# Kernel tuning notes

Hardware: AMD Instinct MI355X
Metric: run time of the kernel (lower is better)

The kernel has to match this reference:

```python
import jax, jax.numpy as jnp
import numpy as np

N_NODES = 500000
N_EDGES = 600000
N_GRAPHS = 4096
X_DIM = 128
H_DIM = 128
Z_DIM = 64
BN_EPS = 1e-5


def setup_inputs() -> dict:
    key = jax.random.key(0)
    ks = jax.random.split(key, 16)
    inp = {
        'x': jax.random.normal(ks[0], (N_NODES, X_DIM), dtype=jnp.float32),
        'edge_index': jax.random.randint(ks[1], (2, N_EDGES), 0, N_NODES),
        'edge_weights': jax.random.uniform(ks[2], (N_EDGES,), dtype=jnp.float32),
        'y_target': jax.random.uniform(ks[3], (N_GRAPHS, 1), dtype=jnp.float32),
        'batch': jnp.sort(jax.random.randint(ks[4], (N_NODES,), 0, N_GRAPHS)),
        # embedder (single weighted GCN-style layer) params
        'W_self': jax.random.normal(ks[5], (X_DIM, H_DIM), dtype=jnp.float32) / np.sqrt(X_DIM),
        'W_nbr': jax.random.normal(ks[6], (X_DIM, H_DIM), dtype=jnp.float32) / np.sqrt(X_DIM),
        'b_emb': jnp.zeros((H_DIM,), dtype=jnp.float32),
        # encoder_mean head: Linear(h_dim+1, z_dim) + BatchNorm1d(z_dim) + ReLU
        'W_mu': jax.random.normal(ks[7], (H_DIM + 1, Z_DIM), dtype=jnp.float32) / np.sqrt(H_DIM + 1),
        'b_mu': jnp.zeros((Z_DIM,), dtype=jnp.float32),
        'gamma_mu': jnp.ones((Z_DIM,), dtype=jnp.float32),
        'beta_mu': jnp.zeros((Z_DIM,), dtype=jnp.float32),
        # encoder_var head: Linear + BN + ReLU + Sigmoid
        'W_var': jax.random.normal(ks[8], (H_DIM + 1, Z_DIM), dtype=jnp.float32) / np.sqrt(H_DIM + 1),
        'b_var': jnp.zeros((Z_DIM,), dtype=jnp.float32),
        'gamma_var': jnp.ones((Z_DIM,), dtype=jnp.float32),
        'beta_var': jnp.zeros((Z_DIM,), dtype=jnp.float32),
    }
    return inp


def _batchnorm(a, gamma, beta):
    # BatchNorm1d in training mode: per-feature batch stats (biased var)
    mu = jnp.mean(a, axis=0, keepdims=True)
    var = jnp.mean((a - mu) ** 2, axis=0, keepdims=True)
    return (a - mu) * jax.lax.rsqrt(var + BN_EPS) * gamma + beta


def reference(x, edge_index, edge_weights, y_target, batch,
              W_self, W_nbr, b_emb,
              W_mu, b_mu, gamma_mu, beta_mu,
              W_var, b_var, gamma_var, beta_var):
    src, dst = edge_index[0], edge_index[1]
    # embedder.embedding(x, edge_index, edge_weights): weighted neighbor agg + self
    msg = jax.ops.segment_sum(edge_weights[:, None] * x[src], dst, num_segments=N_NODES)
    embed = jax.nn.relu(x @ W_self + msg @ W_nbr + b_emb)  # [N, H]
    # global_mean_pool over graph ids
    sums = jax.ops.segment_sum(embed, batch, num_segments=N_GRAPHS)      # [G, H]
    counts = jax.ops.segment_sum(jnp.ones((embed.shape[0],), embed.dtype), batch,
                                 num_segments=N_GRAPHS)
    graph_emb = sums / jnp.maximum(counts, 1.0)[:, None]
    # concat y_target -> [G, H+1]
    h = jnp.concatenate([graph_emb, y_target], axis=1)
    z_mu = jax.nn.relu(_batchnorm(h @ W_mu + b_mu, gamma_mu, beta_mu))
    z_logvar = jax.nn.sigmoid(jax.nn.relu(_batchnorm(h @ W_var + b_var, gamma_var, beta_var)))
    return (z_mu, z_logvar)
```

## Files before the change

kernel.cpp:

```cpp
#include <hip/hip_runtime.h>
#include <hip/hip_bf16.h>
#include <stdint.h>

#define N_NODES 500000
#define N_EDGES 600000
#define N_GRAPHS 4096
#define XD 128
#define HD 128
#define ZD 64
#define BROWS 64
#define NBUCKETS 7813
#define CAP 120

#define OFF_CURS   0ull
#define OFF_SUMS   8192ull
#define OFF_DEG    532480ull
#define OFF_NINFO  1032704ull
#define OFF_CURSOR 1532928ull
#define OFF_SBUF   2033152ull
#define OFF_AT     3909120ull
#define OFF_STATS  4433408ull
#define OFF_WT     4433664ull
#define OFF_GMEAN  4450048ull
#define OFF_PART   4974336ull
#define OFF_PAY    12974848ull

typedef __attribute__((ext_vector_type(8))) short bf16x8;
typedef __attribute__((ext_vector_type(4))) float f32x4;

__device__ inline uint32_t pk_bf16(float lo, float hi) {
  uint32_t ul = __float_as_uint(lo); ul += 0x7fffu + ((ul >> 16) & 1u);
  uint32_t uh = __float_as_uint(hi); uh += 0x7fffu + ((uh >> 16) & 1u);
  return (ul >> 16) | (uh & 0xffff0000u);
}
__device__ inline float bl16(uint32_t u) { return __uint_as_float(u << 16); }
__device__ inline float bh16(uint32_t u) { return __uint_as_float(u & 0xffff0000u); }

__global__ void wprep_kernel(const float* __restrict__ Wnbr, const float* __restrict__ Wself,
                             uint32_t* __restrict__ wt) {
  const float* __restrict__ W = blockIdx.x ? Wself : Wnbr;
  uint32_t* __restrict__ out = wt + (size_t)blockIdx.x * 8192;
  const int t = threadIdx.x;
  const int n = t >> 1, h = t & 1;
  for (int q = 0; q < 32; ++q) {
    int k2 = h * 32 + q;
    float lo = W[(2 * k2) * HD + n];
    float hi = W[(2 * k2 + 1) * HD + n];
    out[n * 64 + k2] = pk_bf16(lo, hi);
  }
}

__global__ void deg_count(const int* __restrict__ ei, uint32_t* __restrict__ deg) {
  int e = blockIdx.x * blockDim.x + threadIdx.x;
  if (e >= N_EDGES) return;
  atomicAdd(deg + ei[N_EDGES + e], 1u);
}

__global__ void scan_prefix(const uint32_t* __restrict__ deg, uint32_t* __restrict__ nodeinfo,
                            uint32_t* __restrict__ cursor) {
  const int b = blockIdx.x;
  const int lane = threadIdx.x;
  int n = b * BROWS + lane;
  int d = (n < N_NODES) ? (int)deg[n] : 0;
  int s = d;
#pragma unroll
  for (int off = 1; off < 64; off <<= 1) {
    int t = __shfl_up(s, off, 64);
    if (lane >= off) s += t;
  }
  int excl = s - d;
  int st = excl < CAP ? excl : CAP;
  int en = (excl + d) < CAP ? (excl + d) : CAP;
  if (n < N_NODES) {
    nodeinfo[n] = (uint32_t)st | ((uint32_t)en << 8);
    cursor[n] = 0u;
  }
}

__global__ void bucket_fill(const int* __restrict__ ei, const float* __restrict__ ew,
                            const uint32_t* __restrict__ nodeinfo, uint32_t* __restrict__ cursor,
                            int* __restrict__ cur_s, uint2* __restrict__ sbuf,
                            uint32_t* __restrict__ payload) {
  int e = blockIdx.x * blockDim.x + threadIdx.x;
  if (e >= N_EDGES) return;
  int src = ei[e];
  int dst = ei[N_EDGES + e];
  float w = ew[e];
  uint32_t info = nodeinfo[dst];
  int st = (int)(info & 0xffu), en = (int)((info >> 8) & 0xffu);
  int slot = (int)atomicAdd(cursor + dst, 1u);
  int pin = st + slot;
  if (pin >= en) return;
  uint32_t pos = (uint32_t)((dst >> 6) * CAP + pin);
  int bs = src >> 6;
  int ss = atomicAdd(cur_s + bs, 1);
  if (ss < CAP) {
    sbuf[(size_t)bs * CAP + ss] =
        make_uint2(((uint32_t)(src & 63) << 20) | pos, __float_as_uint(w));
  } else {
    uint4 z = make_uint4(0, 0, 0, 0);
    uint4* p = (uint4*)((char*)payload + (size_t)pos * 256);
#pragma unroll
    for (int i = 0; i < 16; ++i) p[i] = z;
  }
}

__launch_bounds__(512, 4)
__global__ void gemm_scatter(const float* __restrict__ x, const uint32_t* __restrict__ wt,
                             const uint2* __restrict__ sbuf, const int* __restrict__ cur_s,
                             uint32_t* __restrict__ payload) {
  __shared__ char lb[33728];
  uint2* srec = (uint2*)(lb + 32768);
  const int b = blockIdx.x;
  const int tid = threadIdx.x;
  const int node0 = b * BROWS;
  const int l = tid & 63, w = tid >> 6;
  const int wm = w >> 2, wn = w & 3;
  const int lr = l & 15, lk = l >> 4;

  {
    const int row = tid >> 3, c8 = tid & 7;
    int m = node0 + row;
    int mc = m < N_NODES ? m : N_NODES - 1;
    const float* xr = x + (size_t)mc * XD + c8 * 16;
    uint32_t p[8];
#pragma unroll
    for (int i = 0; i < 4; ++i) {
      float4 t4 = *(const float4*)(xr + i * 4);
      p[2 * i]     = pk_bf16(t4.x, t4.y);
      p[2 * i + 1] = pk_bf16(t4.z, t4.w);
    }
    char* aw = lb + row * 256;
    const int s0 = c8 * 2;
    *(uint4*)(aw + (((s0)     ^ (row & 7)) << 4)) = make_uint4(p[0], p[1], p[2], p[3]);
    *(uint4*)(aw + (((s0 + 1) ^ (row & 7)) << 4)) = make_uint4(p[4], p[5], p[6], p[7]);
  }
  if (tid < CAP) srec[tid] = sbuf[(size_t)b * CAP + tid];
  __syncthreads();

  f32x4 acc0[2][2];
#pragma unroll
  for (int mf = 0; mf < 2; ++mf) { acc0[mf][0] = (f32x4)0.f; acc0[mf][1] = (f32x4)0.f; }

  {
    const char* wtb = (const char*)wt;
#pragma unroll
    for (int kb = 0; kb < 4; ++kb) {
      int slot = (kb << 2) | lk;
      bf16x8 bf0 = *(const bf16x8*)(wtb + (wn * 32 + lr) * 256 + (kb << 6) + (lk << 4));
      bf16x8 bf1 = *(const bf16x8*)(wtb + (wn * 32 + 16 + lr) * 256 + (kb << 6) + (lk << 4));
#pragma unroll
      for (int mf = 0; mf < 2; ++mf) {
        int r = wm * 32 + mf * 16 + lr;
        bf16x8 a = *(const bf16x8*)(lb + r * 256 + ((slot ^ (r & 7)) << 4));
        acc0[mf][0] = __builtin_amdgcn_mfma_f32_16x16x32_bf16(a, bf0, acc0[mf][0], 0, 0, 0);
        acc0[mf][1] = __builtin_amdgcn_mfma_f32_16x16x32_bf16(a, bf1, acc0[mf][1], 0, 0, 0);
      }
    }
  }
  __syncthreads();

  {
#pragma unroll
    for (int mf = 0; mf < 2; ++mf)
#pragma unroll
      for (int nf = 0; nf < 2; ++nf) {
        int col = wn * 32 + nf * 16 + lr;
#pragma unroll
        for (int r = 0; r < 4; ++r) {
          int row = wm * 32 + mf * 16 + lk * 4 + r;
          uint32_t uv = __float_as_uint(acc0[mf][nf][r]);
          uv += 0x7fffu + ((uv >> 16) & 1u);
          *(unsigned short*)(lb + 16384 + row * 256 + ((col * 2) ^ ((row & 7) << 4))) =
              (unsigned short)(uv >> 16);
        }
      }
  }
  __syncthreads();

  {
    int cnt = cur_s[b]; if (cnt > CAP) cnt = CAP;
    const int eg = tid >> 5;
    const int c = tid & 31;
#pragma unroll
    for (int k = 0; k < 8; ++k) {
      int s = eg + (k << 4);
      if (s < cnt) {
        uint2 rec = srec[s];
        int srcloc = (int)(rec.x >> 20);
        uint32_t pos = rec.x & 0xFFFFFu;
        float wgt = __uint_as_float(rec.y);
        uint2 uv = *(const uint2*)(lb + 16384 + srcloc * 256 + ((c * 8) ^ ((srcloc & 7) << 4)));
        float a0 = bl16(uv.x) * wgt, a1 = bh16(uv.x) * wgt;
        float a2 = bl16(uv.y) * wgt, a3 = bh16(uv.y) * wgt;
        *(uint2*)((char*)payload + (size_t)pos * 256 + c * 8) =
            make_uint2(pk_bf16(a0, a1), pk_bf16(a2, a3));
      }
    }
  }
}

__launch_bounds__(512, 3)
__global__ void accum_pool(const float* __restrict__ x, const uint32_t* __restrict__ payload,
                           const uint32_t* __restrict__ nodeinfo,
                           const uint32_t* __restrict__ wt, const float* __restrict__ bemb,
                           const int* __restrict__ batch,
                           float* __restrict__ partials, float* __restrict__ sums) {
  __shared__ float lds[13376];
  float* msg = lds;
  char* astage = (char*)(lds + 8192);
  float* P = lds + 12288;
  int* span = (int*)(lds + 13312);
  const int b = blockIdx.x;
  const int tid = threadIdx.x;
  const int node0 = b * BROWS;
  const int gfirst = batch[node0];
  const int grp = tid >> 5, c = tid & 31;
  const int l = tid & 63, w = tid >> 6;
  const int wm = w >> 2, wn = w & 3;
  const int lr = l & 15, lk = l >> 4;

  for (int i = tid; i < 1024; i += 512) P[i] = 0.f;
  if (tid < 64) {
    int m = node0 + tid;
    span[tid] = (m < N_NODES) ? (batch[m] - gfirst) : -1;
  }

  {
    float acc[4][4];
#pragma unroll
    for (int rr = 0; rr < 4; ++rr)
#pragma unroll
      for (int j = 0; j < 4; ++j) acc[rr][j] = 0.f;

#pragma unroll
    for (int rr = 0; rr < 4; ++rr) {
      int row = grp * 4 + rr;
      int n = node0 + row;
      uint32_t info = (n < N_NODES) ? nodeinfo[n] : 0u;
      int st = (int)(info & 0xffu), en = (int)((info >> 8) & 0xffu);
      for (int i = st; i < en; ++i) {
        uint2 pv = *(const uint2*)(payload + ((size_t)b * CAP + i) * 64 + (c << 1));
        acc[rr][0] += bl16(pv.x);
        acc[rr][1] += bh16(pv.x);
        acc[rr][2] += bl16(pv.y);
        acc[rr][3] += bh16(pv.y);
      }
    }
#pragma unroll
    for (int rr = 0; rr < 4; ++rr) {
      int row = grp * 4 + rr;
      *(float4*)&msg[row * 128 + 4 * (c ^ (row & 7))] =
          make_float4(acc[rr][0], acc[rr][1], acc[rr][2], acc[rr][3]);
    }
  }

  {
    const int row = tid >> 3, c8 = tid & 7;
    int m = node0 + row;
    int mc = m < N_NODES ? m : N_NODES - 1;
    const float* xr = x + (size_t)mc * XD + c8 * 16;
    uint32_t p[8];
#pragma unroll
    for (int i = 0; i < 4; ++i) {
      float4 t4 = *(const float4*)(xr + i * 4);
      p[2 * i]     = pk_bf16(t4.x, t4.y);
      p[2 * i + 1] = pk_bf16(t4.z, t4.w);
    }
    char* aw = astage + row * 256;
    const int s0 = c8 * 2;
    *(uint4*)(aw + (((s0)     ^ (row & 7)) << 4)) = make_uint4(p[0], p[1], p[2], p[3]);
    *(uint4*)(aw + (((s0 + 1) ^ (row & 7)) << 4)) = make_uint4(p[4], p[5], p[6], p[7]);
  }
  __syncthreads();

  f32x4 acc1[2][2];
#pragma unroll
  for (int mf = 0; mf < 2; ++mf) { acc1[mf][0] = (f32x4)0.f; acc1[mf][1] = (f32x4)0.f; }
  {
    const char* wtb = (const char*)wt + 32768;
#pragma unroll
    for (int kb = 0; kb < 4; ++kb) {
      int slot = (kb << 2) | lk;
      bf16x8 bf0 = *(const bf16x8*)(wtb + (wn * 32 + lr) * 256 + (kb << 6) + (lk << 4));
      bf16x8 bf1 = *(const bf16x8*)(wtb + (wn * 32 + 16 + lr) * 256 + (kb << 6) + (lk << 4));
#pragma unroll
      for (int mf = 0; mf < 2; ++mf) {
        int r = wm * 32 + mf * 16 + lr;
        bf16x8 a = *(const bf16x8*)(astage + r * 256 + ((slot ^ (r & 7)) << 4));
        acc1[mf][0] = __builtin_amdgcn_mfma_f32_16x16x32_bf16(a, bf0, acc1[mf][0], 0, 0, 0);
        acc1[mf][1] = __builtin_amdgcn_mfma_f32_16x16x32_bf16(a, bf1, acc1[mf][1], 0, 0, 0);
      }
    }
  }

  {
    float be0 = bemb[wn * 32 + lr];
    float be1 = bemb[wn * 32 + 16 + lr];
#pragma unroll
    for (int mf = 0; mf < 2; ++mf)
#pragma unroll
      for (int r = 0; r < 4; ++r) {
        int row = wm * 32 + mf * 16 + lk * 4 + r;
        int xr = (row & 7) << 2;
        int i0 = row * 128 + ((wn * 32 + lr) ^ xr);
        int i1 = row * 128 + ((wn * 32 + 16 + lr) ^ xr);
        msg[i0] = fmaxf(msg[i0] + acc1[mf][0][r] + be0, 0.f);
        msg[i1] = fmaxf(msg[i1] + acc1[mf][1][r] + be1, 0.f);
      }
  }
  __syncthreads();

  if (tid < 128) {
    const int col = tid;
    float pacc = 0.f;
    int jcur = -1;
    for (int row = 0; row < 64; ++row) {
      int j = span[row];
      if (j != jcur) {
        if (jcur >= 0) {
          if (jcur < 8) P[jcur * 128 + col] = pacc;
          else atomicAdd(&sums[(size_t)(gfirst + jcur) * HD + col], pacc);
        }
        pacc = 0.f; jcur = j;
      }
      if (j >= 0) pacc += msg[row * 128 + (col ^ ((row & 7) << 2))];
    }
    if (jcur >= 0) {
      if (jcur < 8) P[jcur * 128 + col] = pacc;
      else atomicAdd(&sums[(size_t)(gfirst + jcur) * HD + col], pacc);
    }
  }
  __syncthreads();

  {
    float2 v = *(float2*)&P[tid * 2];
    *(float2*)(partials + (size_t)b * 1024 + tid * 2) = v;
  }
}

__global__ void reduce_mean(const float* __restrict__ partials, const float* __restrict__ sums,
                            const int* __restrict__ batch, float* __restrict__ gmean) {
  const int g = blockIdx.x;
  const int t = threadIdx.x;
  int lo = 0, hi = N_NODES;
  while (lo < hi) { int mid = (lo + hi) >> 1; if (batch[mid] < g) lo = mid + 1; else hi = mid; }
  int s = lo; hi = N_NODES;
  while (lo < hi) { int mid = (lo + hi) >> 1; if (batch[mid] < g + 1) lo = mid + 1; else hi = mid; }
  int e = lo;
  float tot = sums[(size_t)g * HD + t];
  int cnt = e - s;
  if (cnt > 0) {
    int b0 = s >> 6, b1 = (e - 1) >> 6;
    for (int b = b0; b <= b1; ++b) {
      int j = g - batch[b * 64];
      if (j >= 0 && j < 8) tot += partials[(size_t)b * 1024 + j * 128 + t];
    }
  }
  gmean[(size_t)g * HD + t] = tot / fmaxf((float)cnt, 1.f);
}

__global__ void head_kernel(const float* __restrict__ gmean, const float* __restrict__ y,
                            const float* __restrict__ Wmu, const float* __restrict__ bmu,
                            const float* __restrict__ Wvar, const float* __restrict__ bvar,
                            float* __restrict__ aT) {
  __shared__ float hrow[129];
  const int g = blockIdx.x;
  const int t = threadIdx.x;
  hrow[t] = gmean[(size_t)g * HD + t];
  if (t == 0) hrow[128] = y[g];
  __syncthreads();
  const int head = t >> 6, n = t & 63;
  const float* __restrict__ W = head ? Wvar : Wmu;
  float acc = head ? bvar[n] : bmu[n];
  for (int k = 0; k < 129; ++k) acc = fmaf(hrow[k], W[k * ZD + n], acc);
  aT[(size_t)(head * ZD + n) * N_GRAPHS + g] = acc;
}

__global__ void bnstats_kernel(const float* __restrict__ aT, float* __restrict__ stats) {
  const int f = blockIdx.x;
  const float* base = aT + (size_t)f * N_GRAPHS;
  float s = 0.f, ss = 0.f;
  for (int i = threadIdx.x; i < N_GRAPHS; i += 256) { float v = base[i]; s += v; ss += v * v; }
#pragma unroll
  for (int off = 1; off < 64; off <<= 1) { s += __shfl_xor(s, off, 64); ss += __shfl_xor(ss, off, 64); }
  __shared__ float ls[8];
  const int wav = threadIdx.x >> 6, lane = threadIdx.x & 63;
  if (lane == 0) { ls[wav * 2] = s; ls[wav * 2 + 1] = ss; }
  __syncthreads();
  if (threadIdx.x == 0) {
    float S = ls[0] + ls[2] + ls[4] + ls[6];
    float SS = ls[1] + ls[3] + ls[5] + ls[7];
    float mean = S / (float)N_GRAPHS;
    float var = SS / (float)N_GRAPHS - mean * mean;
    stats[f * 2] = mean;
    stats[f * 2 + 1] = rsqrtf(var + 1e-5f);
  }
}

__global__ void bnapply_kernel(const float* __restrict__ aT, const float* __restrict__ stats,
                               const float* __restrict__ gm, const float* __restrict__ btm,
                               const float* __restrict__ gv, const float* __restrict__ btv,
                               float* __restrict__ out) {
  int t = blockIdx.x * blockDim.x + threadIdx.x;
  if (t >= 2 * N_GRAPHS * ZD) return;
  int head = t >> 18;
  int r = t & (N_GRAPHS * ZD - 1);
  int g = r >> 6, n = r & 63;
  int f = (head << 6) | n;
  float v = aT[(size_t)f * N_GRAPHS + g];
  float z = (v - stats[f * 2]) * stats[f * 2 + 1];
  z = z * (head ? gv[n] : gm[n]) + (head ? btv[n] : btm[n]);
  z = fmaxf(z, 0.f);
  if (head) z = 1.f / (1.f + __expf(-z));
  out[t] = z;
}

extern "C" void kernel_launch(void* const* d_in, const int* in_sizes, int n_in,
                              void* d_out, int out_size, void* d_ws, size_t ws_size,
                              hipStream_t stream) {
  const float* x      = (const float*)d_in[0];
  const int*   ei     = (const int*)d_in[1];
  const float* ew     = (const float*)d_in[2];
  const float* y      = (const float*)d_in[3];
  const int*   batch  = (const int*)d_in[4];
  const float* Wself  = (const float*)d_in[5];
  const float* Wnbr   = (const float*)d_in[6];
  const float* bemb   = (const float*)d_in[7];
  const float* Wmu    = (const float*)d_in[8];
  const float* bmu    = (const float*)d_in[9];
  const float* gmu    = (const float*)d_in[10];
  const float* betamu = (const float*)d_in[11];
  const float* Wvar   = (const float*)d_in[12];
  const float* bvar   = (const float*)d_in[13];
  const float* gvar   = (const float*)d_in[14];
  const float* betavar= (const float*)d_in[15];

  float* ws         = (float*)d_ws;
  int*   cur_s      = (int*)(ws + OFF_CURS);
  float* sums       = ws + OFF_SUMS;
  uint32_t* deg     = (uint32_t*)(ws + OFF_DEG);
  uint32_t* ninfo   = (uint32_t*)(ws + OFF_NINFO);
  uint32_t* cursor  = (uint32_t*)(ws + OFF_CURSOR);
  uint2* sbuf       = (uint2*)(ws + OFF_SBUF);
  float* aT         = ws + OFF_AT;
  float* stats      = ws + OFF_STATS;
  uint32_t* wt      = (uint32_t*)(ws + OFF_WT);
  float* gmean      = ws + OFF_GMEAN;
  float* partials   = ws + OFF_PART;
  uint32_t* payload = (uint32_t*)(ws + OFF_PAY);

  hipMemsetAsync(ws, 0, (8192ull + 524288ull + 500224ull) * 4ull, stream);

  wprep_kernel<<<2, 256, 0, stream>>>(Wnbr, Wself, wt);
  deg_count<<<(N_EDGES + 255) / 256, 256, 0, stream>>>(ei, deg);
  scan_prefix<<<NBUCKETS, 64, 0, stream>>>(deg, ninfo, cursor);
  bucket_fill<<<(N_EDGES + 255) / 256, 256, 0, stream>>>(ei, ew, ninfo, cursor,
                                                         cur_s, sbuf, payload);
  gemm_scatter<<<NBUCKETS, 512, 0, stream>>>(x, wt, sbuf, cur_s, payload);
  accum_pool<<<NBUCKETS, 512, 0, stream>>>(x, payload, ninfo, wt, bemb, batch,
                                           partials, sums);
  reduce_mean<<<N_GRAPHS, 128, 0, stream>>>(partials, sums, batch, gmean);
  head_kernel<<<N_GRAPHS, 128, 0, stream>>>(gmean, y, Wmu, bmu, Wvar, bvar, aT);
  bnstats_kernel<<<128, 256, 0, stream>>>(aT, stats);
  bnapply_kernel<<<(2 * N_GRAPHS * ZD + 255) / 256, 256, 0, stream>>>(
      aT, stats, gmu, betamu, gvar, betavar, (float*)d_out);
}
```

Baseline: 464.6 us.

## Reorder accum_pool to store GEMM result as bf16 and fuse payload gather into pooling

Removes the fp32 msg LDS buffer. The x@W GEMM output (plus bias) is rounded to bf16 and written back into the input staging buffer. The payload neighbor-message accumulation now runs after the GEMM and feeds straight into ReLU and graph pooling, with all 512 threads sharing the pooling through LDS/global atomics. This cuts LDS use from about 53KB to about 21KB so launch bounds can allow 4 blocks per CU instead of 3. In exchange the pre-activation is rounded to bf16, which costs accuracy, and more atomics are issued.

```diff
diff --git a/kernel.cpp b/kernel.cpp
--- a/kernel.cpp
+++ b/kernel.cpp
@@ -200,17 +200,16 @@
   }
 }
 
-__launch_bounds__(512, 3)
+__launch_bounds__(512, 4)
 __global__ void accum_pool(const float* __restrict__ x, const uint32_t* __restrict__ payload,
                            const uint32_t* __restrict__ nodeinfo,
                            const uint32_t* __restrict__ wt, const float* __restrict__ bemb,
                            const int* __restrict__ batch,
                            float* __restrict__ partials, float* __restrict__ sums) {
-  __shared__ float lds[13376];
-  float* msg = lds;
-  char* astage = (char*)(lds + 8192);
-  float* P = lds + 12288;
-  int* span = (int*)(lds + 13312);
+  __shared__ float lds[5200];
+  char* astage = (char*)lds;
+  float* P = lds + 4096;
+  int* span = (int*)(lds + 5120);
   const int b = blockIdx.x;
   const int tid = threadIdx.x;
   const int node0 = b * BROWS;
@@ -227,35 +226,6 @@
   }
 
   {
-    float acc[4][4];
-#pragma unroll
-    for (int rr = 0; rr < 4; ++rr)
-#pragma unroll
-      for (int j = 0; j < 4; ++j) acc[rr][j] = 0.f;
-
-#pragma unroll
-    for (int rr = 0; rr < 4; ++rr) {
-      int row = grp * 4 + rr;
-      int n = node0 + row;
-      uint32_t info = (n < N_NODES) ? nodeinfo[n] : 0u;
-      int st = (int)(info & 0xffu), en = (int)((info >> 8) & 0xffu);
-      for (int i = st; i < en; ++i) {
-        uint2 pv = *(const uint2*)(payload + ((size_t)b * CAP + i) * 64 + (c << 1));
-        acc[rr][0] += bl16(pv.x);
-        acc[rr][1] += bh16(pv.x);
-        acc[rr][2] += bl16(pv.y);
-        acc[rr][3] += bh16(pv.y);
-      }
-    }
-#pragma unroll
-    for (int rr = 0; rr < 4; ++rr) {
-      int row = grp * 4 + rr;
-      *(float4*)&msg[row * 128 + 4 * (c ^ (row & 7))] =
-          make_float4(acc[rr][0], acc[rr][1], acc[rr][2], acc[rr][3]);
-    }
-  }
-
-  {
     const int row = tid >> 3, c8 = tid & 7;
     int m = node0 + row;
     int mc = m < N_NODES ? m : N_NODES - 1;
@@ -293,6 +263,7 @@
       }
     }
   }
+  __syncthreads();
 
   {
     float be0 = bemb[wn * 32 + lr];
@@ -300,35 +271,72 @@
 #pragma unroll
     for (int mf = 0; mf < 2; ++mf)
 #pragma unroll
-      for (int r = 0; r < 4; ++r) {
-        int row = wm * 32 + mf * 16 + lk * 4 + r;
-        int xr = (row & 7) << 2;
-        int i0 = row * 128 + ((wn * 32 + lr) ^ xr);
-        int i1 = row * 128 + ((wn * 32 + 16 + lr) ^ xr);
-        msg[i0] = fmaxf(msg[i0] + acc1[mf][0][r] + be0, 0.f);
-        msg[i1] = fmaxf(msg[i1] + acc1[mf][1][r] + be1, 0.f);
-      }
-  }
-  __syncthreads();
-
-  if (tid < 128) {
-    const int col = tid;
-    float pacc = 0.f;
+      for (int nf = 0; nf < 2; ++nf) {
+        int col = wn * 32 + nf * 16 + lr;
+        float be = nf ? be1 : be0;
+#pragma unroll
+        for (int r = 0; r < 4; ++r) {
+          int row = wm * 32 + mf * 16 + lk * 4 + r;
+          uint32_t uv = __float_as_uint(acc1[mf][nf][r] + be);
+          uv += 0x7fffu + ((uv >> 16) & 1u);
+          *(unsigned short*)(astage + row * 256 + ((col * 2) ^ ((row & 7) << 4))) =
+              (unsigned short)(uv >> 16);
+        }
+      }
+  }
+  __syncthreads();
+
+  {
+    float p0 = 0.f, p1 = 0.f, p2 = 0.f, p3 = 0.f;
     int jcur = -1;
-    for (int row = 0; row < 64; ++row) {
+#pragma unroll
+    for (int rr = 0; rr < 4; ++rr) {
+      int row = grp * 4 + rr;
+      int n = node0 + row;
       int j = span[row];
-      if (j != jcur) {
-        if (jcur >= 0) {
-          if (jcur < 8) P[jcur * 128 + col] = pacc;
-          else atomicAdd(&sums[(size_t)(gfirst + jcur) * HD + col], pacc);
+      float a0 = 0.f, a1 = 0.f, a2 = 0.f, a3 = 0.f;
+      uint32_t info = (n < N_NODES) ? nodeinfo[n] : 0u;
+      int st = (int)(info & 0xffu), en = (int)((info >> 8) & 0xffu);
+      for (int i = st; i < en; ++i) {
+        uint2 pv = *(const uint2*)(payload + ((size_t)b * CAP + i) * 64 + (c << 1));
+        a0 += bl16(pv.x); a1 += bh16(pv.x);
+        a2 += bl16(pv.y); a3 += bh16(pv.y);
+      }
+      if (j >= 0) {
+        uint2 vv = *(const uint2*)(astage + row * 256 + ((c * 8) ^ ((row & 7) << 4)));
+        float z0 = fmaxf(a0 + bl16(vv.x), 0.f);
+        float z1 = fmaxf(a1 + bh16(vv.x), 0.f);
+        float z2 = fmaxf(a2 + bl16(vv.y), 0.f);
+        float z3 = fmaxf(a3 + bh16(vv.y), 0.f);
+        if (j != jcur) {
+          if (jcur >= 0) {
+            if (jcur < 8) {
+              atomicAdd(&P[jcur * 128 + 4 * c + 0], p0);
+              atomicAdd(&P[jcur * 128 + 4 * c + 1], p1);
+              atomicAdd(&P[jcur * 128 + 4 * c + 2], p2);
+              atomicAdd(&P[jcur * 128 + 4 * c + 3], p3);
+            } else {
+              float* sp = sums + (size_t)(gfirst + jcur) * HD + 4 * c;
+              atomicAdd(sp + 0, p0); atomicAdd(sp + 1, p1);
+              atomicAdd(sp + 2, p2); atomicAdd(sp + 3, p3);
+            }
+          }
+          p0 = p1 = p2 = p3 = 0.f; jcur = j;
         }
-        pacc = 0.f; jcur = j;
-      }
-      if (j >= 0) pacc += msg[row * 128 + (col ^ ((row & 7) << 2))];
+        p0 += z0; p1 += z1; p2 += z2; p3 += z3;
+      }
     }
     if (jcur >= 0) {
-      if (jcur < 8) P[jcur * 128 + col] = pacc;
-      else atomicAdd(&sums[(size_t)(gfirst + jcur) * HD + col], pacc);
+      if (jcur < 8) {
+        atomicAdd(&P[jcur * 128 + 4 * c + 0], p0);
+        atomicAdd(&P[jcur * 128 + 4 * c + 1], p1);
+        atomicAdd(&P[jcur * 128 + 4 * c + 2], p2);
+        atomicAdd(&P[jcur * 128 + 4 * c + 3], p3);
+      } else {
+        float* sp = sums + (size_t)(gfirst + jcur) * HD + 4 * c;
+        atomicAdd(sp + 0, p0); atomicAdd(sp + 1, p1);
+        atomicAdd(sp + 2, p2); atomicAdd(sp + 3, p3);
+      }
     }
   }
   __syncthreads();
```

Measured after the change: 432.6 us. 1.07x faster.
